# Kernel optimization log

Hardware: AMD Instinct MI355X
Metric: run time of the kernel (lower is better)

Reference implementation:

```python
import jax, jax.numpy as jnp
import numpy as np
from jax import lax

B_, CIN, COUT, H, W = 8, 64, 64, 64, 64
DIN, DSTATE, K, DTRANK = 128, 16, 4, 4  # d_inner=2*C, d_state=16, 4 scan dirs, dt_rank=ceil(64/16)


def setup_inputs():
    key = jax.random.key(0)
    ks = jax.random.split(key, 10)
    f = lambda k, s, sc=0.02: jax.random.normal(k, s, jnp.float32) * sc
    return {
        "x": jax.random.normal(ks[0], (B_, CIN, H, W), jnp.float32),
        "conv_w": f(ks[1], (COUT, CIN, 3, 3)),
        "conv_b": jnp.zeros((COUT,), jnp.float32),
        "gn_g": jnp.ones((COUT,), jnp.float32),
        "gn_b": jnp.zeros((COUT,), jnp.float32),
        "ln1_g": jnp.ones((COUT,), jnp.float32),
        "ln1_b": jnp.zeros((COUT,), jnp.float32),
        "in_proj_w": f(ks[2], (COUT, 2 * DIN)),
        "dw_w": f(ks[3], (DIN, 1, 3, 3)),
        "dw_b": jnp.zeros((DIN,), jnp.float32),
        "x_proj_w": f(ks[4], (K, DTRANK + 2 * DSTATE, DIN)),
        "dt_w": f(ks[5], (K, DIN, DTRANK)),
        "dt_b": f(ks[6], (K, DIN), 0.01),
        "A_logs": jnp.tile(jnp.log(jnp.arange(1, DSTATE + 1, dtype=jnp.float32)), (K, DIN, 1)),
        "Ds": jnp.ones((K, DIN), jnp.float32),
        "out_norm_g": jnp.ones((DIN,), jnp.float32),
        "out_norm_b": jnp.zeros((DIN,), jnp.float32),
        "out_proj_w": f(ks[7], (DIN, COUT)),
    }


def _ln(x, g, b, eps=1e-5):
    m = x.mean(-1, keepdims=True)
    v = ((x - m) ** 2).mean(-1, keepdims=True)
    return (x - m) * lax.rsqrt(v + eps) * g + b


def reference(x, conv_w, conv_b, gn_g, gn_b, ln1_g, ln1_b, in_proj_w, dw_w, dw_b,
              x_proj_w, dt_w, dt_b, A_logs, Ds, out_norm_g, out_norm_b, out_proj_w):
    # BasicConv2d: conv3x3 (stride 1, pad 1) + GroupNorm(2) + SiLU
    y = lax.conv_general_dilated(x, conv_w, (1, 1), [(1, 1), (1, 1)],
                                 dimension_numbers=("NCHW", "OIHW", "NCHW"))
    y = y + conv_b[None, :, None, None]
    Bb, C, Hh, Ww = y.shape
    yg = y.reshape(Bb, 2, C // 2, Hh, Ww)
    m = yg.mean((2, 3, 4), keepdims=True)
    v = ((yg - m) ** 2).mean((2, 3, 4), keepdims=True)
    y = ((yg - m) * lax.rsqrt(v + 1e-5)).reshape(Bb, C, Hh, Ww)
    y = y * gn_g[None, :, None, None] + gn_b[None, :, None, None]
    y = jax.nn.silu(y)
    # VSSBlock on NHWC: LN -> SS2D -> residual
    xb = y.transpose(0, 2, 3, 1)                       # (B,H,W,C)
    h = _ln(xb, ln1_g, ln1_b)
    xz = h @ in_proj_w                                 # (B,H,W,2*DIN)
    xm, z = jnp.split(xz, 2, axis=-1)
    xm = xm.transpose(0, 3, 1, 2)                      # (B,DIN,H,W)
    xm = lax.conv_general_dilated(xm, dw_w, (1, 1), [(1, 1), (1, 1)],
                                  dimension_numbers=("NCHW", "OIHW", "NCHW"),
                                  feature_group_count=DIN)
    xm = jax.nn.silu(xm + dw_b[None, :, None, None])
    L = Hh * Ww
    x1 = xm.reshape(Bb, DIN, L)                        # HW order
    x2 = xm.transpose(0, 1, 3, 2).reshape(Bb, DIN, L)  # WH order
    xs = jnp.stack([x1, x2], 1)
    xs = jnp.concatenate([xs, jnp.flip(xs, -1)], 1)    # (B,4,DIN,L)
    xdbl = jnp.einsum("bkdl,kcd->bkcl", xs, x_proj_w)
    dts, Bs, Cs = jnp.split(xdbl, [DTRANK, DTRANK + DSTATE], axis=2)
    dts = jnp.einsum("bkrl,kdr->bkdl", dts, dt_w)
    dt = jax.nn.softplus(dts + dt_b[None, :, :, None])  # (B,4,DIN,L)
    A = -jnp.exp(A_logs)                                # (K,DIN,DSTATE)
    # selective scan over L (time-major)
    u_t = xs.transpose(3, 0, 1, 2)
    dt_t = dt.transpose(3, 0, 1, 2)
    B_t = Bs.transpose(3, 0, 1, 2)
    C_t = Cs.transpose(3, 0, 1, 2)

    def step(hst, inp):
        u, d, Bc, Cc = inp
        hst = hst * jnp.exp(d[..., None] * A) + (d * u)[..., None] * Bc[:, :, None, :]
        return hst, jnp.einsum("bkdn,bkn->bkd", hst, Cc)

    h0 = jnp.zeros((Bb, K, DIN, DSTATE), xs.dtype)
    _, ys = lax.scan(step, h0, (u_t, dt_t, B_t, C_t))  # ys: (L,B,4,DIN)
    out_y = ys.transpose(1, 2, 3, 0) + Ds[None, :, :, None] * xs
    inv_y = jnp.flip(out_y[:, 2:4], -1)
    wh_y = out_y[:, 1].reshape(Bb, DIN, Ww, Hh).transpose(0, 1, 3, 2).reshape(Bb, DIN, L)
    invwh_y = inv_y[:, 1].reshape(Bb, DIN, Ww, Hh).transpose(0, 1, 3, 2).reshape(Bb, DIN, L)
    yv = out_y[:, 0] + inv_y[:, 0] + wh_y + invwh_y    # (B,DIN,L)
    yv = yv.transpose(0, 2, 1).reshape(Bb, Hh, Ww, DIN)
    yv = _ln(yv, out_norm_g, out_norm_b)
    yv = yv * jax.nn.silu(z)
    vss = xb + yv @ out_proj_w                          # VSSBlock residual
    return vss.transpose(0, 3, 1, 2) + y                # MambaDU residual
```

## Files before the change

### kernel.cpp

```cpp
#include <hip/hip_runtime.h>
#include <hip/hip_bf16.h>

#define BD   8
#define CD   64
#define HD   64
#define WD   64
#define LD   4096
#define DINN 128
#define KDIR 4
#define NST  16
#define L2E  1.442695040888963f

typedef const float* fp;

__device__ __forceinline__ float sigm(float x) { return 1.f / (1.f + __expf(-x)); }
__device__ __forceinline__ float softplusf(float x) {
    float e = __expf(-fabsf(x));
    return fmaxf(x, 0.f) + __logf(1.f + e);
}
__device__ __forceinline__ int pmap(int k, int l) {
    int m = (k & 2) ? (LD - 1 - l) : l;
    return (k & 1) ? (((m & 63) << 6) | (m >> 6)) : m;
}

__global__ __launch_bounds__(256) void k_wt(fp cw, float* wt) {
    int id = blockIdx.x * 256 + threadIdx.x;
    if (id >= 64 * 64 * 9) return;
    int co = id & 63; int ciq = id >> 6; int ci = ciq / 9; int q = ciq % 9;
    wt[id] = cw[(co * 64 + ci) * 9 + q];
}

__global__ __launch_bounds__(256) void k_conv(fp x, const float* wt, fp cb, float* conv_out, float* gstats) {
    __shared__ float xt[64][3][68];
    __shared__ float red[4][4];
    int bx = blockIdx.x; int b = bx >> 6; int h = bx & 63;
    int t = threadIdx.x;
    for (int idx = t; idx < 64 * 3 * 64; idx += 256) {
        int ci = idx / 192, rem = idx % 192, r = rem >> 6, w = rem & 63;
        int hs = h + r - 1;
        float v = 0.f;
        if (hs >= 0 && hs < 64) v = x[((b * 64 + ci) * 64 + hs) * 64 + w];
        xt[ci][r][w + 1] = v;
    }
    for (int idx = t; idx < 64 * 3; idx += 256) {
        int ci = idx / 3, r = idx % 3;
        xt[ci][r][0] = 0.f; xt[ci][r][65] = 0.f; xt[ci][r][66] = 0.f; xt[ci][r][67] = 0.f;
    }
    __syncthreads();
    int coq = t & 15, wq = t >> 4;
    float acc[4][4];
#pragma unroll
    for (int c = 0; c < 4; c++)
#pragma unroll
        for (int j = 0; j < 4; j++) acc[c][j] = 0.f;
    for (int ci = 0; ci < 64; ci++) {
        float4 wv[9];
#pragma unroll
        for (int q = 0; q < 9; q++) wv[q] = *(const float4*)&wt[(ci * 9 + q) * 64 + coq * 4];
#pragma unroll
        for (int r = 0; r < 3; r++) {
            const float* row = &xt[ci][r][wq * 4];
            float4 f0 = ((const float4*)row)[0], f1 = ((const float4*)row)[1];
            float xr[8] = {f0.x, f0.y, f0.z, f0.w, f1.x, f1.y, f1.z, f1.w};
            float4 wa = wv[r * 3 + 0], wb = wv[r * 3 + 1], wc = wv[r * 3 + 2];
#pragma unroll
            for (int j = 0; j < 4; j++) {
                acc[0][j] += wa.x * xr[j] + wb.x * xr[j + 1] + wc.x * xr[j + 2];
                acc[1][j] += wa.y * xr[j] + wb.y * xr[j + 1] + wc.y * xr[j + 2];
                acc[2][j] += wa.z * xr[j] + wb.z * xr[j + 1] + wc.z * xr[j + 2];
                acc[3][j] += wa.w * xr[j] + wb.w * xr[j + 1] + wc.w * xr[j + 2];
            }
        }
    }
    float ps0 = 0.f, pq0 = 0.f, ps1 = 0.f, pq1 = 0.f;
    bool g0 = coq < 8;
#pragma unroll
    for (int cc = 0; cc < 4; cc++) {
        int co = coq * 4 + cc;
        float bias = cb[co];
        float4 o;
        o.x = acc[cc][0] + bias; o.y = acc[cc][1] + bias;
        o.z = acc[cc][2] + bias; o.w = acc[cc][3] + bias;
        *(float4*)&conv_out[((b * 64 + co) * 64 + h) * 64 + wq * 4] = o;
        float s = o.x + o.y + o.z + o.w;
        float q2 = o.x * o.x + o.y * o.y + o.z * o.z + o.w * o.w;
        if (g0) { ps0 += s; pq0 += q2; } else { ps1 += s; pq1 += q2; }
    }
#pragma unroll
    for (int off = 32; off; off >>= 1) {
        ps0 += __shfl_xor(ps0, off); pq0 += __shfl_xor(pq0, off);
        ps1 += __shfl_xor(ps1, off); pq1 += __shfl_xor(pq1, off);
    }
    int wid = t >> 6;
    if ((t & 63) == 0) { red[wid][0] = ps0; red[wid][1] = pq0; red[wid][2] = ps1; red[wid][3] = pq1; }
    __syncthreads();
    if (t < 4) {
        float v = red[0][t] + red[1][t] + red[2][t] + red[3][t];
        atomicAdd(&gstats[b * 4 + t], v);
    }
}

__global__ __launch_bounds__(256) void k_gnapply(const float* conv_out, const float* gstats,
                                                 fp gng, fp gnb, float* y_nhwc) {
    __shared__ float tile[64][65];
    int bx = blockIdx.x; int b = bx >> 6; int p0 = (bx & 63) * 64;
    int t = threadIdx.x;
    const float invN = 1.f / (32.f * 4096.f);
    float s0 = gstats[b * 4 + 0], q0 = gstats[b * 4 + 1];
    float s1 = gstats[b * 4 + 2], q1 = gstats[b * 4 + 3];
    float m0 = s0 * invN, r0 = rsqrtf(q0 * invN - m0 * m0 + 1e-5f);
    float m1 = s1 * invN, r1 = rsqrtf(q1 * invN - m1 * m1 + 1e-5f);
    for (int idx = t; idx < 4096; idx += 256) {
        int c = idx >> 6, pi = idx & 63;
        float v = conv_out[(b * 64 + c) * LD + p0 + pi];
        float mean = (c < 32) ? m0 : m1, rstd = (c < 32) ? r0 : r1;
        v = (v - mean) * rstd * gng[c] + gnb[c];
        v = v * sigm(v);
        tile[c][pi] = v;
    }
    __syncthreads();
    for (int idx = t; idx < 4096; idx += 256) {
        int pi = idx >> 6, c = idx & 63;
        y_nhwc[(b * LD + p0 + pi) * 64 + c] = tile[c][pi];
    }
}

__global__ __launch_bounds__(256) void k_lninproj(const float* y_nhwc, fp lng, fp lnb, fp ipw,
                                                  float* xmc, float* zsil) {
    __shared__ float hn[4][64];
    int bp0 = blockIdx.x * 4;
    int t = threadIdx.x;
    int pix = t >> 6, lane = t & 63;
    {
        float v = y_nhwc[(bp0 + pix) * 64 + lane];
        float s = v, s2 = v * v;
#pragma unroll
        for (int off = 32; off; off >>= 1) { s += __shfl_xor(s, off); s2 += __shfl_xor(s2, off); }
        float mean = s * (1.f / 64.f);
        float rstd = rsqrtf(s2 * (1.f / 64.f) - mean * mean + 1e-5f);
        hn[pix][lane] = (v - mean) * rstd * lng[lane] + lnb[lane];
    }
    __syncthreads();
    float a0 = 0.f, a1 = 0.f, a2 = 0.f, a3 = 0.f;
    for (int c = 0; c < 64; c++) {
        float w = ipw[c * 256 + t];
        a0 += hn[0][c] * w; a1 += hn[1][c] * w; a2 += hn[2][c] * w; a3 += hn[3][c] * w;
    }
    float accv[4] = {a0, a1, a2, a3};
#pragma unroll
    for (int p = 0; p < 4; p++) {
        int bp = bp0 + p;
        float v = accv[p];
        if (t < 128) xmc[bp * 128 + t] = v;
        else         zsil[bp * 128 + (t - 128)] = v * sigm(v);
    }
}

__global__ __launch_bounds__(256) void k_dwconv(const float* xmc, fp dww, fp dwb, float* xm_dw) {
    int id = blockIdx.x * 256 + threadIdx.x;
    int d = id & 127, p = (id >> 7) & (LD - 1), b = id >> 19;
    int h = p >> 6, w = p & 63;
    float wv[9];
#pragma unroll
    for (int q = 0; q < 9; q++) wv[q] = dww[d * 9 + q];
    float acc = dwb[d];
#pragma unroll
    for (int i = 0; i < 3; i++) {
        int hs = h + i - 1; if (hs < 0 || hs > 63) continue;
#pragma unroll
        for (int j = 0; j < 3; j++) {
            int ws = w + j - 1; if (ws < 0 || ws > 63) continue;
            acc += xmc[((b << 12) + (hs << 6) + ws) * 128 + d] * wv[i * 3 + j];
        }
    }
    acc = acc * sigm(acc);
    xm_dw[id] = acc;
}

__global__ __launch_bounds__(192) void k_proj(const float* xm_dw, fp xpw, float* dts4, float* xBC) {
    __shared__ float u_lds[64 * 130];
    __shared__ float w_lds[128 * 40];
    int bx = blockIdx.x;
    int lt = bx & 63; int bk = bx >> 6; int k = bk & 3; int b = bk >> 2;
    int l0 = lt * 64;
    int t = threadIdx.x;
    for (int idx = t; idx < 36 * 128; idx += 192) {
        int c = idx % 36, d = idx / 36;
        w_lds[d * 40 + c] = xpw[(k * 36 + c) * 128 + d];
    }
    for (int idx = t; idx < 64 * 128; idx += 192) {
        int l = idx >> 7, d = idx & 127;
        u_lds[l * 130 + d] = xm_dw[(b * LD + pmap(k, l0 + l)) * 128 + d];
    }
    __syncthreads();
    int l = t & 63, cg = t >> 6;
    float acc[12];
#pragma unroll
    for (int i = 0; i < 12; i++) acc[i] = 0.f;
    for (int d = 0; d < 128; d++) {
        float uv = u_lds[l * 130 + d];
        const float* wr = &w_lds[d * 40 + cg * 12];
#pragma unroll
        for (int q = 0; q < 3; q++) {
            float4 f = ((const float4*)wr)[q];
            acc[4 * q + 0] += f.x * uv;
            acc[4 * q + 1] += f.y * uv;
            acc[4 * q + 2] += f.z * uv;
            acc[4 * q + 3] += f.w * uv;
        }
    }
    int base = bk * LD + l0 + l;
#pragma unroll
    for (int i = 0; i < 12; i++) {
        int c = cg * 12 + i;
        if (c < 4) dts4[base * 4 + c] = acc[i];
        else       xBC[base * 32 + (c - 4)] = acc[i];
    }
}

__global__ __launch_bounds__(128) void k_scan1(const float* xm_dw, const float* dts4, const float* xBC,
                                               fp dtw, fp dtbp, fp alog,
                                               float* Pbuf, float* Hbuf, int NCr, int CLr) {
    __shared__ float s_b[64 * 16];
    __shared__ float s_d4[64 * 4];
    int c = blockIdx.x, k = blockIdx.y, b = blockIdx.z;
    int d = threadIdx.x;
    int bk = b * 4 + k;
    int kd = k * 128 + d;
    float w0 = dtw[kd * 4 + 0], w1 = dtw[kd * 4 + 1], w2 = dtw[kd * 4 + 2], w3 = dtw[kd * 4 + 3];
    float dtb = dtbp[kd];
    float base = -__expf(alog[kd * 16]) * L2E;
    float A2[16];
    bool geo = true;
#pragma unroll
    for (int n = 0; n < 16; n++) {
        A2[n] = -__expf(alog[kd * 16 + n]) * L2E;
        float ideal = (float)(n + 1) * base;
        geo = geo && (fabsf(A2[n] - ideal) <= 1e-4f * fabsf(ideal));
    }
    float h[16]; float sdt = 0.f;
#pragma unroll
    for (int n = 0; n < 16; n++) h[n] = 0.f;
    int l0 = c * CLr;
    for (int ss = 0; ss < CLr; ss += 64) {
        if (ss) __syncthreads();
        int ls = l0 + ss;
        const float4* gd = (const float4*)&dts4[(size_t)(bk * LD + ls) * 4];
        if (d < 64) ((float4*)s_d4)[d] = gd[d];
        const float4* gx = (const float4*)&xBC[(size_t)(bk * LD + ls) * 32];
        for (int i = d; i < 64 * 4; i += 128) { int s = i >> 2, q = i & 3; ((float4*)s_b)[i] = gx[s * 8 + q]; }
        __syncthreads();
        int pbase = pmap(k, ls);
        int pstep = pmap(k, ls + 1) - pbase;
        const float* up = xm_dw + (size_t)(b * LD + pbase) * 128 + d;
        long ustep = (long)pstep * 128;
        if (geo) {
#pragma unroll 4
            for (int s = 0; s < 64; s++) {
                float4 dv = ((const float4*)s_d4)[s];
                float dtv = softplusf(dv.x * w0 + dv.y * w1 + dv.z * w2 + dv.w * w3 + dtb);
                sdt += dtv;
                float u = *up; up += ustep;
                float du = dtv * u;
                const float4* Bp = (const float4*)&s_b[s * 16];
                float4 B0 = Bp[0], B1 = Bp[1], B2 = Bp[2], B3 = Bp[3];
                float r = exp2f(dtv * base);
                float r2 = r * r, r3 = r2 * r, r4 = r2 * r2;
                float r5 = r4 * r, r6 = r4 * r2, r7 = r4 * r3, r8 = r4 * r4;
                float r9 = r8 * r, r10 = r8 * r2, r11 = r8 * r3, r12 = r8 * r4;
                float r13 = r8 * r5, r14 = r8 * r6, r15 = r8 * r7, r16 = r8 * r8;
                h[0]  = r   * h[0]  + du * B0.x;  h[1]  = r2  * h[1]  + du * B0.y;
                h[2]  = r3  * h[2]  + du * B0.z;  h[3]  = r4  * h[3]  + du * B0.w;
                h[4]  = r5  * h[4]  + du * B1.x;  h[5]  = r6  * h[5]  + du * B1.y;
                h[6]  = r7  * h[6]  + du * B1.z;  h[7]  = r8  * h[7]  + du * B1.w;
                h[8]  = r9  * h[8]  + du * B2.x;  h[9]  = r10 * h[9]  + du * B2.y;
                h[10] = r11 * h[10] + du * B2.z;  h[11] = r12 * h[11] + du * B2.w;
                h[12] = r13 * h[12] + du * B3.x;  h[13] = r14 * h[13] + du * B3.y;
                h[14] = r15 * h[14] + du * B3.z;  h[15] = r16 * h[15] + du * B3.w;
            }
        } else {
#pragma unroll 2
            for (int s = 0; s < 64; s++) {
                float4 dv = ((const float4*)s_d4)[s];
                float dtv = softplusf(dv.x * w0 + dv.y * w1 + dv.z * w2 + dv.w * w3 + dtb);
                sdt += dtv;
                float u = *up; up += ustep;
                float du = dtv * u;
                const float* Bp = &s_b[s * 16];
#pragma unroll
                for (int n = 0; n < 16; n++) {
                    float a = exp2f(dtv * A2[n]);
                    h[n] = a * h[n] + du * Bp[n];
                }
            }
        }
    }
    int obase = (bk * NCr + c) * 2048 + d;
#pragma unroll
    for (int n = 0; n < 16; n++) {
        Pbuf[obase + n * 128] = exp2f(sdt * A2[n]);
        Hbuf[obase + n * 128] = h[n];
    }
}

__global__ __launch_bounds__(256) void k_scan2(const float* Pbuf, const float* Hbuf, float* Hinit, int NCr) {
    int id = blockIdx.x * 256 + threadIdx.x;
    int nd = id & 2047; int bk = id >> 11;
    float h = 0.f;
    int base = bk * NCr * 2048 + nd;
    for (int c = 0; c < NCr; c++) {
        int idx = base + c * 2048;
        Hinit[idx] = h;
        h = Hbuf[idx] + Pbuf[idx] * h;
    }
}

__global__ __launch_bounds__(128) void k_scan3(const float* xm_dw, const float* dts4, const float* xBC,
                                               fp dtw, fp dtbp, fp alog, fp dsp,
                                               const float* Hinit, float* yv, int NCr, int CLr) {
    __shared__ float s_bc[64 * 32];
    __shared__ float s_d4[64 * 4];
    int c = blockIdx.x, k = blockIdx.y, b = blockIdx.z;
    int d = threadIdx.x;
    int bk = b * 4 + k;
    int kd = k * 128 + d;
    float w0 = dtw[kd * 4 + 0], w1 = dtw[kd * 4 + 1], w2 = dtw[kd * 4 + 2], w3 = dtw[kd * 4 + 3];
    float dtb = dtbp[kd];
    float Dv = dsp[kd];
    float base = -__expf(alog[kd * 16]) * L2E;
    float A2[16];
    bool geo = true;
#pragma unroll
    for (int n = 0; n < 16; n++) {
        A2[n] = -__expf(alog[kd * 16 + n]) * L2E;
        float ideal = (float)(n + 1) * base;
        geo = geo && (fabsf(A2[n] - ideal) <= 1e-4f * fabsf(ideal));
    }
    int hbase = (bk * NCr + c) * 2048 + d;
    float h[16];
#pragma unroll
    for (int n = 0; n < 16; n++) h[n] = Hinit[hbase + n * 128];
    int l0 = c * CLr;
    for (int ss = 0; ss < CLr; ss += 64) {
        if (ss) __syncthreads();
        int ls = l0 + ss;
        const float4* gd = (const float4*)&dts4[(size_t)(bk * LD + ls) * 4];
        if (d < 64) ((float4*)s_d4)[d] = gd[d];
        const float4* gx = (const float4*)&xBC[(size_t)(bk * LD + ls) * 32];
        for (int i = d; i < 64 * 8; i += 128) ((float4*)s_bc)[i] = gx[i];
        __syncthreads();
        int pbase = pmap(k, ls);
        int pstep = pmap(k, ls + 1) - pbase;
        const float* up = xm_dw + (size_t)(b * LD + pbase) * 128 + d;
        float* yp = yv + (size_t)(b * LD + pbase) * 128 + d;
        long ustep = (long)pstep * 128;
        if (geo) {
#pragma unroll 4
            for (int s = 0; s < 64; s++) {
                float4 dv = ((const float4*)s_d4)[s];
                float dtv = softplusf(dv.x * w0 + dv.y * w1 + dv.z * w2 + dv.w * w3 + dtb);
                float u = *up; up += ustep;
                float du = dtv * u;
                const float4* Bp = (const float4*)&s_bc[s * 32];
                float4 B0 = Bp[0], B1 = Bp[1], B2 = Bp[2], B3 = Bp[3];
                float4 C0 = Bp[4], C1 = Bp[5], C2 = Bp[6], C3 = Bp[7];
                float r = exp2f(dtv * base);
                float r2 = r * r, r3 = r2 * r, r4 = r2 * r2;
                float r5 = r4 * r, r6 = r4 * r2, r7 = r4 * r3, r8 = r4 * r4;
                float r9 = r8 * r, r10 = r8 * r2, r11 = r8 * r3, r12 = r8 * r4;
                float r13 = r8 * r5, r14 = r8 * r6, r15 = r8 * r7, r16 = r8 * r8;
                float y;
                h[0]  = r   * h[0]  + du * B0.x;  y  = h[0]  * C0.x;
                h[1]  = r2  * h[1]  + du * B0.y;  y += h[1]  * C0.y;
                h[2]  = r3  * h[2]  + du * B0.z;  y += h[2]  * C0.z;
                h[3]  = r4  * h[3]  + du * B0.w;  y += h[3]  * C0.w;
                h[4]  = r5  * h[4]  + du * B1.x;  y += h[4]  * C1.x;
                h[5]  = r6  * h[5]  + du * B1.y;  y += h[5]  * C1.y;
                h[6]  = r7  * h[6]  + du * B1.z;  y += h[6]  * C1.z;
                h[7]  = r8  * h[7]  + du * B1.w;  y += h[7]  * C1.w;
                h[8]  = r9  * h[8]  + du * B2.x;  y += h[8]  * C2.x;
                h[9]  = r10 * h[9]  + du * B2.y;  y += h[9]  * C2.y;
                h[10] = r11 * h[10] + du * B2.z;  y += h[10] * C2.z;
                h[11] = r12 * h[11] + du * B2.w;  y += h[11] * C2.w;
                h[12] = r13 * h[12] + du * B3.x;  y += h[12] * C3.x;
                h[13] = r14 * h[13] + du * B3.y;  y += h[13] * C3.y;
                h[14] = r15 * h[14] + du * B3.z;  y += h[14] * C3.z;
                h[15] = r16 * h[15] + du * B3.w;  y += h[15] * C3.w;
                y += Dv * u;
                atomicAdd(yp, y); yp += ustep;
            }
        } else {
#pragma unroll 2
            for (int s = 0; s < 64; s++) {
                float4 dv = ((const float4*)s_d4)[s];
                float dtv = softplusf(dv.x * w0 + dv.y * w1 + dv.z * w2 + dv.w * w3 + dtb);
                float u = *up; up += ustep;
                float du = dtv * u;
                const float* Bp = &s_bc[s * 32];
                float y = 0.f;
#pragma unroll
                for (int n = 0; n < 16; n++) {
                    float a = exp2f(dtv * A2[n]);
                    h[n] = a * h[n] + du * Bp[n];
                    y += h[n] * Bp[16 + n];
                }
                y += Dv * u;
                atomicAdd(yp, y); yp += ustep;
            }
        }
    }
}

__global__ __launch_bounds__(256) void k_final(const float* yv, const float* zsil, const float* y_nhwc,
                                               fp ong, fp onb, fp opw, float* out) {
    __shared__ float ylds[2][128];
    __shared__ float red[2][2][2];
    __shared__ float part[2][2][64];
    int bp0 = blockIdx.x * 2;
    int t = threadIdx.x;
    int pix = t >> 7, tl = t & 127;
    int bp = bp0 + pix;
    float v = yv[bp * 128 + tl];
    float s = v, s2 = v * v;
#pragma unroll
    for (int off = 32; off; off >>= 1) { s += __shfl_xor(s, off); s2 += __shfl_xor(s2, off); }
    int wh = (t >> 6) & 1;
    if ((t & 63) == 0) { red[pix][wh][0] = s; red[pix][wh][1] = s2; }
    __syncthreads();
    float S = red[pix][0][0] + red[pix][1][0], S2 = red[pix][0][1] + red[pix][1][1];
    float mean = S * (1.f / 128.f);
    float rstd = rsqrtf(S2 * (1.f / 128.f) - mean * mean + 1e-5f);
    float vn = (v - mean) * rstd * ong[tl] + onb[tl];
    vn *= zsil[bp * 128 + tl];
    ylds[pix][tl] = vn;
    __syncthreads();
    {
        int px = t >> 7, half = (t >> 6) & 1, co = t & 63;
        float acc = 0.f;
        const float* yrow = &ylds[px][half * 64];
        const float* wcol = &opw[half * 64 * 64 + co];
#pragma unroll 16
        for (int dd = 0; dd < 64; dd++) acc += yrow[dd] * wcol[dd * 64];
        part[px][half][co] = acc;
    }
    __syncthreads();
    if (t < 128) {
        int pp = t >> 6, co = t & 63;
        int bpo = bp0 + pp;
        float a = part[pp][0][co] + part[pp][1][co];
        float yb = y_nhwc[bpo * 64 + co];
        out[((bpo >> 12) * 64 + co) * LD + (bpo & 4095)] = 2.f * yb + a;
    }
}

extern "C" void kernel_launch(void* const* d_in, const int* in_sizes, int n_in,
                              void* d_out, int out_size, void* d_ws, size_t ws_size,
                              hipStream_t stream) {
    fp x    = (fp)d_in[0];
    fp cw   = (fp)d_in[1];
    fp cb   = (fp)d_in[2];
    fp gng  = (fp)d_in[3];
    fp gnb  = (fp)d_in[4];
    fp lng  = (fp)d_in[5];
    fp lnb  = (fp)d_in[6];
    fp ipw  = (fp)d_in[7];
    fp dww  = (fp)d_in[8];
    fp dwb  = (fp)d_in[9];
    fp xpw  = (fp)d_in[10];
    fp dtw  = (fp)d_in[11];
    fp dtb  = (fp)d_in[12];
    fp alog = (fp)d_in[13];
    fp dsp  = (fp)d_in[14];
    fp ong  = (fp)d_in[15];
    fp onb  = (fp)d_in[16];
    fp opw  = (fp)d_in[17];

    float* w = (float*)d_ws;
    float* conv_out = w;  w += BD * 64 * LD;
    float* y_nhwc   = w;  w += BD * LD * 64;
    float* gstats   = w;  w += 32;
    float* wt       = w;  w += 64 * 64 * 9;
    float* xmc      = w;  w += BD * LD * 128;
    float* zsil     = w;  w += BD * LD * 128;
    float* xm_dw    = w;  w += BD * LD * 128;
    float* dts4     = w;  w += BD * KDIR * LD * 4;
    float* xBC      = w;  w += BD * KDIR * LD * 32;
    float* yv       = w;  w += BD * LD * 128;
    size_t base_floats = (size_t)(w - (float*)d_ws);

    int NCr = 32;
    size_t perbuf64 = (size_t)32 * 64 * 2048;
    float *Pbuf, *Hbuf, *Hinit;
    if (ws_size >= (base_floats + 3 * perbuf64) * sizeof(float)) {
        NCr = 64;
        Pbuf  = w;  w += perbuf64;
        Hbuf  = w;  w += perbuf64;
        Hinit = w;  w += perbuf64;
    } else {
        Pbuf  = xmc;
        Hbuf  = xmc + (size_t)32 * 32 * 2048;
        Hinit = conv_out;
    }
    int CLr = LD / NCr;
    if (ws_size < base_floats * sizeof(float)) return;

    hipMemsetAsync(gstats, 0, 32 * sizeof(float), stream);
    k_wt<<<144, 256, 0, stream>>>(cw, wt);
    k_conv<<<BD * HD, 256, 0, stream>>>(x, wt, cb, conv_out, gstats);
    k_gnapply<<<BD * 64, 256, 0, stream>>>(conv_out, gstats, gng, gnb, y_nhwc);
    k_lninproj<<<BD * LD / 4, 256, 0, stream>>>(y_nhwc, lng, lnb, ipw, xmc, zsil);
    k_dwconv<<<BD * LD * 128 / 256, 256, 0, stream>>>(xmc, dww, dwb, xm_dw);
    k_proj<<<BD * KDIR * 64, 192, 0, stream>>>(xm_dw, xpw, dts4, xBC);
    k_scan1<<<dim3(NCr, KDIR, BD), 128, 0, stream>>>(xm_dw, dts4, xBC, dtw, dtb, alog, Pbuf, Hbuf, NCr, CLr);
    k_scan2<<<256, 256, 0, stream>>>(Pbuf, Hbuf, Hinit, NCr);
    hipMemsetAsync(yv, 0, (size_t)BD * LD * 128 * sizeof(float), stream);
    k_scan3<<<dim3(NCr, KDIR, BD), 128, 0, stream>>>(xm_dw, dts4, xBC, dtw, dtb, alog, dsp, Hinit, yv, NCr, CLr);
    k_final<<<BD * LD / 2, 256, 0, stream>>>(yv, zsil, y_nhwc, ong, onb, opw, (float*)d_out);
}
```

Before: 452.6 us.

## Split conv input channels across two blocks and move GroupNorm stats to separate kernel

```diff
diff --git a/kernel.cpp b/kernel.cpp
--- a/kernel.cpp
+++ b/kernel.cpp
@@ -30,20 +30,25 @@
     wt[id] = cw[(co * 64 + ci) * 9 + q];
 }
 
-__global__ __launch_bounds__(256) void k_conv(fp x, const float* wt, fp cb, float* conv_out, float* gstats) {
-    __shared__ float xt[64][3][68];
-    __shared__ float red[4][4];
-    int bx = blockIdx.x; int b = bx >> 6; int h = bx & 63;
+__global__ __launch_bounds__(256, 4) void k_conv(fp x, const float* wt, fp cb,
+                                                 float* out0, float* out1) {
+    __shared__ float xt[32][3][68];
+    int bx = blockIdx.x;
+    int half = bx & 1; int bh = bx >> 1; int h = bh & 63; int b = bh >> 6;
     int t = threadIdx.x;
-    for (int idx = t; idx < 64 * 3 * 64; idx += 256) {
-        int ci = idx / 192, rem = idx % 192, r = rem >> 6, w = rem & 63;
+    int ci0 = half << 5;
+#pragma unroll
+    for (int r = 0; r < 3; r++) {
         int hs = h + r - 1;
-        float v = 0.f;
-        if (hs >= 0 && hs < 64) v = x[((b * 64 + ci) * 64 + hs) * 64 + w];
-        xt[ci][r][w + 1] = v;
-    }
-    for (int idx = t; idx < 64 * 3; idx += 256) {
-        int ci = idx / 3, r = idx % 3;
+        bool ok = (hs >= 0 && hs < 64);
+        const float* xrow = x + (((size_t)b * 64 + ci0) * 64 + (ok ? hs : 0)) * 64;
+        for (int s = t; s < 2048; s += 256) {
+            int ci = s >> 6, w = s & 63;
+            xt[ci][r][w + 1] = ok ? xrow[ci * 4096 + w] : 0.f;
+        }
+    }
+    for (int s = t; s < 96; s += 256) {
+        int ci = s / 3, r = s - ci * 3;
         xt[ci][r][0] = 0.f; xt[ci][r][65] = 0.f; xt[ci][r][66] = 0.f; xt[ci][r][67] = 0.f;
     }
     __syncthreads();
@@ -53,10 +58,12 @@
     for (int c = 0; c < 4; c++)
 #pragma unroll
         for (int j = 0; j < 4; j++) acc[c][j] = 0.f;
-    for (int ci = 0; ci < 64; ci++) {
+
+    const float* wbase = wt + (size_t)ci0 * 9 * 64 + coq * 4;
+    for (int ci = 0; ci < 32; ci++) {
         float4 wv[9];
 #pragma unroll
-        for (int q = 0; q < 9; q++) wv[q] = *(const float4*)&wt[(ci * 9 + q) * 64 + coq * 4];
+        for (int q = 0; q < 9; q++) wv[q] = *(const float4*)&wbase[(ci * 9 + q) * 64];
 #pragma unroll
         for (int r = 0; r < 3; r++) {
             const float* row = &xt[ci][r][wq * 4];
@@ -72,35 +79,46 @@
             }
         }
     }
-    float ps0 = 0.f, pq0 = 0.f, ps1 = 0.f, pq1 = 0.f;
-    bool g0 = coq < 8;
+    float* dst = half ? out1 : out0;
 #pragma unroll
     for (int cc = 0; cc < 4; cc++) {
         int co = coq * 4 + cc;
-        float bias = cb[co];
+        float bias = half ? 0.f : cb[co];
         float4 o;
         o.x = acc[cc][0] + bias; o.y = acc[cc][1] + bias;
         o.z = acc[cc][2] + bias; o.w = acc[cc][3] + bias;
-        *(float4*)&conv_out[((b * 64 + co) * 64 + h) * 64 + wq * 4] = o;
-        float s = o.x + o.y + o.z + o.w;
-        float q2 = o.x * o.x + o.y * o.y + o.z * o.z + o.w * o.w;
-        if (g0) { ps0 += s; pq0 += q2; } else { ps1 += s; pq1 += q2; }
-    }
-#pragma unroll
-    for (int off = 32; off; off >>= 1) {
-        ps0 += __shfl_xor(ps0, off); pq0 += __shfl_xor(pq0, off);
-        ps1 += __shfl_xor(ps1, off); pq1 += __shfl_xor(pq1, off);
-    }
+        *(float4*)&dst[((b * 64 + co) * 64 + h) * 64 + wq * 4] = o;
+    }
+}
+
+__global__ __launch_bounds__(256) void k_gnstats2(const float* c0, const float* c1, float* gstats) {
+    int bx = blockIdx.x;
+    int slice = bx & 31; int bg = bx >> 5; int g = bg & 1; int b = bg >> 1;
+    int t = threadIdx.x;
+    size_t base = ((size_t)(b * 64 + g * 32 + slice)) * 4096;
+    const float4* p0 = (const float4*)(c0 + base);
+    const float4* p1 = (const float4*)(c1 + base);
+    float s = 0.f, s2 = 0.f;
+#pragma unroll
+    for (int i = 0; i < 4; i++) {
+        float4 a = p0[t + i * 256], bv = p1[t + i * 256];
+        float vx = a.x + bv.x, vy = a.y + bv.y, vz = a.z + bv.z, vw = a.w + bv.w;
+        s += vx + vy + vz + vw;
+        s2 += vx * vx + vy * vy + vz * vz + vw * vw;
+    }
+#pragma unroll
+    for (int off = 32; off; off >>= 1) { s += __shfl_xor(s, off); s2 += __shfl_xor(s2, off); }
+    __shared__ float rs[4], rq[4];
     int wid = t >> 6;
-    if ((t & 63) == 0) { red[wid][0] = ps0; red[wid][1] = pq0; red[wid][2] = ps1; red[wid][3] = pq1; }
-    __syncthreads();
-    if (t < 4) {
-        float v = red[0][t] + red[1][t] + red[2][t] + red[3][t];
-        atomicAdd(&gstats[b * 4 + t], v);
-    }
-}
-
-__global__ __launch_bounds__(256) void k_gnapply(const float* conv_out, const float* gstats,
+    if ((t & 63) == 0) { rs[wid] = s; rq[wid] = s2; }
+    __syncthreads();
+    if (t == 0) {
+        atomicAdd(&gstats[b * 4 + g * 2 + 0], rs[0] + rs[1] + rs[2] + rs[3]);
+        atomicAdd(&gstats[b * 4 + g * 2 + 1], rq[0] + rq[1] + rq[2] + rq[3]);
+    }
+}
+
+__global__ __launch_bounds__(256) void k_gnapply(const float* c0, const float* c1, const float* gstats,
                                                  fp gng, fp gnb, float* y_nhwc) {
     __shared__ float tile[64][65];
     int bx = blockIdx.x; int b = bx >> 6; int p0 = (bx & 63) * 64;
@@ -112,7 +130,8 @@
     float m1 = s1 * invN, r1 = rsqrtf(q1 * invN - m1 * m1 + 1e-5f);
     for (int idx = t; idx < 4096; idx += 256) {
         int c = idx >> 6, pi = idx & 63;
-        float v = conv_out[(b * 64 + c) * LD + p0 + pi];
+        size_t gi = (size_t)(b * 64 + c) * LD + p0 + pi;
+        float v = c0[gi] + c1[gi];
         float mean = (c < 32) ? m0 : m1, rstd = (c < 32) ? r0 : r1;
         v = (v - mean) * rstd * gng[c] + gnb[c];
         v = v * sigm(v);
@@ -476,16 +495,17 @@
     fp opw  = (fp)d_in[17];
 
     float* w = (float*)d_ws;
-    float* conv_out = w;  w += BD * 64 * LD;
-    float* y_nhwc   = w;  w += BD * LD * 64;
-    float* gstats   = w;  w += 32;
-    float* wt       = w;  w += 64 * 64 * 9;
-    float* xmc      = w;  w += BD * LD * 128;
-    float* zsil     = w;  w += BD * LD * 128;
-    float* xm_dw    = w;  w += BD * LD * 128;
-    float* dts4     = w;  w += BD * KDIR * LD * 4;
-    float* xBC      = w;  w += BD * KDIR * LD * 32;
-    float* yv       = w;  w += BD * LD * 128;
+    float* conv_out0 = w;  w += BD * 64 * LD;
+    float* conv_out1 = w;  w += BD * 64 * LD;
+    float* y_nhwc    = w;  w += BD * LD * 64;
+    float* gstats    = w;  w += 32;
+    float* wt        = w;  w += 64 * 64 * 9;
+    float* xmc       = w;  w += BD * LD * 128;
+    float* zsil      = w;  w += BD * LD * 128;
+    float* xm_dw     = w;  w += BD * LD * 128;
+    float* dts4      = w;  w += BD * KDIR * LD * 4;
+    float* xBC       = w;  w += BD * KDIR * LD * 32;
+    float* yv        = w;  w += BD * LD * 128;
     size_t base_floats = (size_t)(w - (float*)d_ws);
 
     int NCr = 32;
@@ -499,15 +519,16 @@
     } else {
         Pbuf  = xmc;
         Hbuf  = xmc + (size_t)32 * 32 * 2048;
-        Hinit = conv_out;
+        Hinit = conv_out0;
     }
     int CLr = LD / NCr;
     if (ws_size < base_floats * sizeof(float)) return;
 
     hipMemsetAsync(gstats, 0, 32 * sizeof(float), stream);
     k_wt<<<144, 256, 0, stream>>>(cw, wt);
-    k_conv<<<BD * HD, 256, 0, stream>>>(x, wt, cb, conv_out, gstats);
-    k_gnapply<<<BD * 64, 256, 0, stream>>>(conv_out, gstats, gng, gnb, y_nhwc);
+    k_conv<<<BD * HD * 2, 256, 0, stream>>>(x, wt, cb, conv_out0, conv_out1);
+    k_gnstats2<<<BD * 2 * 32, 256, 0, stream>>>(conv_out0, conv_out1, gstats);
+    k_gnapply<<<BD * 64, 256, 0, stream>>>(conv_out0, conv_out1, gstats, gng, gnb, y_nhwc);
     k_lninproj<<<BD * LD / 4, 256, 0, stream>>>(y_nhwc, lng, lnb, ipw, xmc, zsil);
     k_dwconv<<<BD * LD * 128 / 256, 256, 0, stream>>>(xmc, dww, dwb, xm_dw);
     k_proj<<<BD * KDIR * 64, 192, 0, stream>>>(xm_dw, xpw, dts4, xBC);
```

Result: no change. 445.0 us (-1.7%).
